# Kernel tuning notes

Hardware: AMD Instinct MI355X
Metric: run time of the kernel (lower is better)

Reference implementation:

```python
import jax, jax.numpy as jnp
import numpy as np

N = 8192

def setup_inputs() -> dict:
    key = jax.random.key(0)
    k1, k2, k3, k4, k5, k6 = jax.random.split(key, 6)
    return {
        "t": jnp.zeros((), dtype=jnp.float32),
        "state": jax.random.uniform(k1, (3 * N,), dtype=jnp.float32),
        "betas": jax.random.uniform(k2, (N,), dtype=jnp.float32),
        "deltas": jax.random.uniform(k3, (N,), dtype=jnp.float32),
        "cs": jax.random.uniform(k4, (N,), dtype=jnp.float32),
        "ps": jax.random.uniform(k5, (N,), dtype=jnp.float32),
        "ts": jax.random.uniform(k6, (N, N), dtype=jnp.float32) * 0.5,
    }

def reference(t, state, betas, deltas, cs, ps, ts):
    # squared parametrization of all learned params
    T = jnp.square(ts)                      # [N, N]
    diag = jnp.diagonal(T)                  # T[n, n]
    row_sum = jnp.sum(T, axis=1)            # sum over T[n, :]
    # normalization[n] = min(T[n,n] / (sum_k T[n,k] - T[n,n]), 1)
    norm = jnp.minimum(diag / (row_sum - diag), jnp.float32(1.0))

    s = state.reshape(-1, 3)                # [N, 3] -> (U, I, V) per host
    U, I, V = s[:, 0], s[:, 1], s[:, 2]

    b2 = jnp.square(betas)
    d2 = jnp.square(deltas)
    p2 = jnp.square(ps)
    c2 = jnp.square(cs)

    bUV = b2 * U * V
    dU = -bUV
    dI = bUV - d2 * I
    # coupling[n] = sum_{nbr != n} norm[nbr] * T[nbr, n] * V[nbr]
    coupling = (norm * V) @ T - norm * diag * V
    dV = p2 * I - c2 * V - diag + coupling

    return jnp.stack([dU, dI, dV], axis=1).reshape(-1)
```

## Files before the change

kernel.cpp:

```cpp
#include <hip/hip_runtime.h>

#define NN 8192
#define CHUNKS 128
#define CHUNK_ROWS (NN / CHUNKS)
#define COLTILES 8


__global__ void __launch_bounds__(256)
row_pass(const float* __restrict__ ts,
         const float* __restrict__ state,
         float* __restrict__ w,
         float* __restrict__ diag_out) {
    const int row = blockIdx.x;
    const float4* rowp = reinterpret_cast<const float4*>(ts + (size_t)row * NN);
    float sum = 0.f;
    #pragma unroll
    for (int k = threadIdx.x; k < NN / 4; k += 256) {
        float4 v = rowp[k];
        sum += v.x * v.x + v.y * v.y + v.z * v.z + v.w * v.w;
    }
    #pragma unroll
    for (int off = 32; off; off >>= 1) sum += __shfl_down(sum, off);
    __shared__ float red[4];
    const int lane = threadIdx.x & 63;
    const int wid  = threadIdx.x >> 6;
    if (lane == 0) red[wid] = sum;
    __syncthreads();
    if (threadIdx.x == 0) {
        float total = red[0] + red[1] + red[2] + red[3];
        float d = ts[(size_t)row * NN + row];
        d = d * d;
        const float norm = fminf(d / (total - d), 1.0f);
        w[row]        = norm * state[3 * row + 2];
        diag_out[row] = d;
    }
}

__global__ void __launch_bounds__(256)
col_pass(const float* __restrict__ ts,
         const float* __restrict__ w,
         float* __restrict__ partial) {
    __shared__ float wsm[CHUNK_ROWS];
    const int row0 = blockIdx.y * CHUNK_ROWS;
    if (threadIdx.x < CHUNK_ROWS) wsm[threadIdx.x] = w[row0 + threadIdx.x];
    __syncthreads();

    const int col = blockIdx.x * 1024 + threadIdx.x * 4;
    const float* base = ts + (size_t)row0 * NN + col;
    float4 acc = {0.f, 0.f, 0.f, 0.f};
    #pragma unroll 8
    for (int r = 0; r < CHUNK_ROWS; ++r) {
        const float wi = wsm[r];
        float4 v = *reinterpret_cast<const float4*>(base + (size_t)r * NN);
        acc.x += wi * v.x * v.x;
        acc.y += wi * v.y * v.y;
        acc.z += wi * v.z * v.z;
        acc.w += wi * v.w * v.w;
    }
    *reinterpret_cast<float4*>(partial + (size_t)blockIdx.y * NN + col) = acc;
}

__global__ void __launch_bounds__(256)
finalize(const float* __restrict__ state,
         const float* __restrict__ betas,
         const float* __restrict__ deltas,
         const float* __restrict__ cs,
         const float* __restrict__ ps,
         const float* __restrict__ w,
         const float* __restrict__ diag,
         const float* __restrict__ partial,
         float* __restrict__ out) {
    const int j = blockIdx.x * 256 + threadIdx.x;
    float coup = 0.f;
    #pragma unroll 8
    for (int c = 0; c < CHUNKS; ++c) coup += partial[(size_t)c * NN + j];
    const float dj = diag[j];
    coup -= w[j] * dj;

    const float U = state[3 * j + 0];
    const float I = state[3 * j + 1];
    const float V = state[3 * j + 2];
    const float b2 = betas[j] * betas[j];
    const float d2 = deltas[j] * deltas[j];
    const float p2 = ps[j] * ps[j];
    const float c2 = cs[j] * cs[j];
    const float bUV = b2 * U * V;

    out[3 * j + 0] = -bUV;
    out[3 * j + 1] = bUV - d2 * I;
    out[3 * j + 2] = p2 * I - c2 * V - dj + coup;
}

extern "C" void kernel_launch(void* const* d_in, const int* in_sizes, int n_in,
                              void* d_out, int out_size, void* d_ws, size_t ws_size,
                              hipStream_t stream) {
    const float* state  = (const float*)d_in[1];
    const float* betas  = (const float*)d_in[2];
    const float* deltas = (const float*)d_in[3];
    const float* cs     = (const float*)d_in[4];
    const float* ps     = (const float*)d_in[5];
    const float* ts     = (const float*)d_in[6];
    float* out = (float*)d_out;

    float* w       = (float*)d_ws;
    float* diag    = w + NN;
    float* partial = diag + NN;

    row_pass<<<NN, 256, 0, stream>>>(ts, state, w, diag);

    dim3 g2(COLTILES, CHUNKS);
    col_pass<<<g2, 256, 0, stream>>>(ts, w, partial);

    finalize<<<NN / 256, 256, 0, stream>>>(state, betas, deltas, cs, ps,
                                           w, diag, partial, out);
}
```

Baseline: 416.1 us.

## Fuse row-norm and column accumulation into a single pass over ts

```diff
diff --git a/kernel.cpp b/kernel.cpp
--- a/kernel.cpp
+++ b/kernel.cpp
@@ -1,63 +1,88 @@
 #include <hip/hip_runtime.h>
 
 #define NN 8192
-#define CHUNKS 128
-#define CHUNK_ROWS (NN / CHUNKS)
-#define COLTILES 8
+#define RPB 8
+#define NBLK (NN / RPB)
+#define SUB 4
 
 
-__global__ void __launch_bounds__(256)
-row_pass(const float* __restrict__ ts,
-         const float* __restrict__ state,
-         float* __restrict__ w,
-         float* __restrict__ diag_out) {
-    const int row = blockIdx.x;
-    const float4* rowp = reinterpret_cast<const float4*>(ts + (size_t)row * NN);
-    float sum = 0.f;
+__global__ void __launch_bounds__(256, 4)
+main_pass(const float* __restrict__ ts,
+          const float* __restrict__ state,
+          float* __restrict__ wv,
+          float* __restrict__ diag,
+          float* __restrict__ partial)
+{
+    __shared__ float acc[NN];
+    __shared__ float wrow[SUB];
+
+    const int tid  = threadIdx.x;
+    const int lane = tid & 63;
+    const int wid  = tid >> 6;
+
     #pragma unroll
-    for (int k = threadIdx.x; k < NN / 4; k += 256) {
-        float4 v = rowp[k];
-        sum += v.x * v.x + v.y * v.y + v.z * v.z + v.w * v.w;
+    for (int i = tid; i < NN; i += 256) acc[i] = 0.f;
+
+    const int row0 = blockIdx.x * RPB;
+
+    for (int s = 0; s < RPB / SUB; ++s) {
+        const int r = row0 + s * SUB + wid;
+        const float* rp = ts + (size_t)r * NN;
+        float sum = 0.f;
+        const float4* rp4 = (const float4*)rp;
+        #pragma unroll 8
+        for (int it = 0; it < 32; ++it) {
+            float4 v = rp4[lane + it * 64];
+            sum += v.x * v.x + v.y * v.y + v.z * v.z + v.w * v.w;
+        }
+        #pragma unroll
+        for (int off = 32; off; off >>= 1) sum += __shfl_down(sum, off);
+        if (lane == 0) {
+            float d = rp[r]; d *= d;
+            const float nrm = fminf(d / (sum - d), 1.0f);
+            const float wr  = nrm * state[3 * r + 2];
+            wrow[wid] = wr;
+            wv[r]     = wr;
+            diag[r]   = d;
+        }
+        __syncthreads();
+        const int colBase = wid * 2048;
+        for (int rr = 0; rr < SUB; ++rr) {
+            const float wr = wrow[rr];
+            const float4* rq = (const float4*)(ts + (size_t)(row0 + s * SUB + rr) * NN + colBase);
+            #pragma unroll 8
+            for (int it = 0; it < 8; ++it) {
+                const int idx = lane + it * 64;
+                float4 v = rq[idx];
+                float4* a = (float4*)&acc[colBase + idx * 4];
+                float4 av = *a;
+                av.x += wr * v.x * v.x;
+                av.y += wr * v.y * v.y;
+                av.z += wr * v.z * v.z;
+                av.w += wr * v.w * v.w;
+                *a = av;
+            }
+        }
+        __syncthreads();
     }
+    float* pout = partial + (size_t)blockIdx.x * NN;
     #pragma unroll
-    for (int off = 32; off; off >>= 1) sum += __shfl_down(sum, off);
-    __shared__ float red[4];
-    const int lane = threadIdx.x & 63;
-    const int wid  = threadIdx.x >> 6;
-    if (lane == 0) red[wid] = sum;
-    __syncthreads();
-    if (threadIdx.x == 0) {
-        float total = red[0] + red[1] + red[2] + red[3];
-        float d = ts[(size_t)row * NN + row];
-        d = d * d;
-        const float norm = fminf(d / (total - d), 1.0f);
-        w[row]        = norm * state[3 * row + 2];
-        diag_out[row] = d;
-    }
+    for (int i = tid; i < NN / 4; i += 256)
+        ((float4*)pout)[i] = ((const float4*)acc)[i];
 }
 
 __global__ void __launch_bounds__(256)
-col_pass(const float* __restrict__ ts,
-         const float* __restrict__ w,
-         float* __restrict__ partial) {
-    __shared__ float wsm[CHUNK_ROWS];
-    const int row0 = blockIdx.y * CHUNK_ROWS;
-    if (threadIdx.x < CHUNK_ROWS) wsm[threadIdx.x] = w[row0 + threadIdx.x];
-    __syncthreads();
-
+reduce1(const float* __restrict__ partial, float* __restrict__ partial2)
+{
     const int col = blockIdx.x * 1024 + threadIdx.x * 4;
-    const float* base = ts + (size_t)row0 * NN + col;
+    const float* base = partial + (size_t)blockIdx.y * 32 * NN + col;
     float4 acc = {0.f, 0.f, 0.f, 0.f};
     #pragma unroll 8
-    for (int r = 0; r < CHUNK_ROWS; ++r) {
-        const float wi = wsm[r];
-        float4 v = *reinterpret_cast<const float4*>(base + (size_t)r * NN);
-        acc.x += wi * v.x * v.x;
-        acc.y += wi * v.y * v.y;
-        acc.z += wi * v.z * v.z;
-        acc.w += wi * v.w * v.w;
+    for (int k = 0; k < 32; ++k) {
+        float4 v = *(const float4*)(base + (size_t)k * NN);
+        acc.x += v.x; acc.y += v.y; acc.z += v.z; acc.w += v.w;
     }
-    *reinterpret_cast<float4*>(partial + (size_t)blockIdx.y * NN + col) = acc;
+    *(float4*)(partial2 + (size_t)blockIdx.y * NN + col) = acc;
 }
 
 __global__ void __launch_bounds__(256)
@@ -66,16 +91,17 @@
          const float* __restrict__ deltas,
          const float* __restrict__ cs,
          const float* __restrict__ ps,
-         const float* __restrict__ w,
+         const float* __restrict__ wv,
          const float* __restrict__ diag,
-         const float* __restrict__ partial,
-         float* __restrict__ out) {
+         const float* __restrict__ partial2,
+         float* __restrict__ out)
+{
     const int j = blockIdx.x * 256 + threadIdx.x;
     float coup = 0.f;
     #pragma unroll 8
-    for (int c = 0; c < CHUNKS; ++c) coup += partial[(size_t)c * NN + j];
+    for (int k = 0; k < 32; ++k) coup += partial2[(size_t)k * NN + j];
     const float dj = diag[j];
-    coup -= w[j] * dj;
+    coup -= wv[j] * dj;
 
     const float U = state[3 * j + 0];
     const float I = state[3 * j + 1];
@@ -102,15 +128,13 @@
     const float* ts     = (const float*)d_in[6];
     float* out = (float*)d_out;
 
-    float* w       = (float*)d_ws;
-    float* diag    = w + NN;
-    float* partial = diag + NN;
+    float* wv       = (float*)d_ws;
+    float* diag     = wv + NN;
+    float* partial  = diag + NN;
+    float* partial2 = partial + (size_t)NBLK * NN;
 
-    row_pass<<<NN, 256, 0, stream>>>(ts, state, w, diag);
-
-    dim3 g2(COLTILES, CHUNKS);
-    col_pass<<<g2, 256, 0, stream>>>(ts, w, partial);
-
+    main_pass<<<NBLK, 256, 0, stream>>>(ts, state, wv, diag, partial);
+    reduce1<<<dim3(8, 32), 256, 0, stream>>>(partial, partial2);
     finalize<<<NN / 256, 256, 0, stream>>>(state, betas, deltas, cs, ps,
-                                           w, diag, partial, out);
+                                           wv, diag, partial2, out);
 }
```

After: 410.1 us. Within noise of the previous version (-1.4%).
